# Performance work log

Hardware: AMD Instinct MI355X
Metric: run time of the kernel (lower is better)

The kernel has to match this reference:

```python
import jax, jax.numpy as jnp
import numpy as np

DN = ('NCDHW', 'OIDHW', 'NCDHW')
HIDDEN = 512
VOCAB = 8192


def conv3d_s122(x, w, b):
    # stride (1,2,2), padding 1 on all three spatial-temporal dims
    y = jax.lax.conv_general_dilated(x, w, window_strides=(1, 2, 2),
                                     padding=[(1, 1), (1, 1), (1, 1)],
                                     dimension_numbers=DN)
    return y + b[None, :, None, None, None]


def setup_inputs() -> dict:
    key = jax.random.key(0)
    ks = jax.random.split(key, 9)
    c1, c2 = HIDDEN // 4, HIDDEN // 2
    inp = {
        'video': jax.random.normal(ks[0], (2, 3, 16, 128, 128), dtype=jnp.float32),
        'w1': jax.random.normal(ks[1], (c1, 3, 3, 3, 3), dtype=jnp.float32) * 0.05,
        'b1': jnp.zeros((c1,), dtype=jnp.float32),
        'w2': jax.random.normal(ks[2], (c2, c1, 3, 3, 3), dtype=jnp.float32) * 0.05,
        'b2': jnp.zeros((c2,), dtype=jnp.float32),
        'w3': jax.random.normal(ks[3], (HIDDEN, c2, 3, 3, 3), dtype=jnp.float32) * 0.05,
        'b3': jnp.zeros((HIDDEN,), dtype=jnp.float32),
        'codebook': jax.random.normal(ks[4], (VOCAB, HIDDEN), dtype=jnp.float32),
        'emb_table': jax.random.normal(ks[5], (VOCAB, HIDDEN), dtype=jnp.float32),
        'resolution_level': 0,
    }
    return inp


def reference(video, w1, b1, w2, b2, w3, b3, codebook, emb_table, resolution_level):
    h = jax.nn.relu(conv3d_s122(video, w1, b1))
    h = jax.nn.relu(conv3d_s122(h, w2, b2))
    f = conv3d_s122(h, w3, b3)                       # [B, C, T, H', W']
    B, C = f.shape[0], f.shape[1]
    feats = f.reshape(B, C, -1).transpose(0, 2, 1)   # [B, N, C]
    # squared L2 distances (argmin identical to cdist's sqrt distances)
    f2 = jnp.sum(feats * feats, axis=-1, keepdims=True)          # [B, N, 1]
    c2 = jnp.sum(codebook * codebook, axis=-1)                   # [V]
    dots = jnp.einsum('bnc,vc->bnv', feats, codebook)            # [B, N, V]
    sqdist = f2 + c2[None, None, :] - 2.0 * dots
    tokens = jnp.argmin(sqdist, axis=-1)                         # [B, N] int
    embeddings = emb_table[tokens]                               # [B, N, C]
    return tokens, embeddings
```

## Files before the change

### kernel.cpp

```cpp
#include <hip/hip_runtime.h>

typedef __bf16 bf16x8 __attribute__((ext_vector_type(8)));
typedef float  f32x4  __attribute__((ext_vector_type(4)));

__device__ __forceinline__ unsigned int splitpack(float x) {
  unsigned int u = __float_as_uint(x);
  unsigned int hi = (u + 0x7fffu + ((u >> 16) & 1u)) >> 16;
  float l = x - __uint_as_float(hi << 16);
  unsigned int ul = __float_as_uint(l);
  unsigned int lo = (ul + 0x7fffu + ((ul >> 16) & 1u)) >> 16;
  return hi | (lo << 16);
}

__device__ __forceinline__ void mfma_bf16(f32x4& d, uint4 a, uint4 b) {
  d = __builtin_amdgcn_mfma_f32_16x16x32_bf16(
        __builtin_bit_cast(bf16x8, a), __builtin_bit_cast(bf16x8, b), d, 0, 0, 0);
}

__device__ __forceinline__ void glds16(const void* g, void* l) {
  __builtin_amdgcn_global_load_lds(
      (const __attribute__((address_space(1))) unsigned int*)g,
      (__attribute__((address_space(3))) unsigned int*)l, 16, 0, 0);
}


__global__ void conv1_k(const float* __restrict__ in, const float* __restrict__ wgt,
                        const float* __restrict__ bias,
                        unsigned short* __restrict__ h1h, unsigned short* __restrict__ h1l) {
  const int tx = threadIdx.x;
  const int w0 = tx * 4;
  const int h  = blockIdx.x * 16 + threadIdx.y;
  const int co0 = blockIdx.y * 8;
  const int bz = blockIdx.z;
  const int b = bz >> 4, t = bz & 15;

  float acc[8][4];
  #pragma unroll
  for (int i = 0; i < 8; ++i) {
    const float bv = bias[co0 + i];
    #pragma unroll
    for (int j = 0; j < 4; ++j) acc[i][j] = bv;
  }
  const int cs = 2 * w0 - 2;

  for (int ci = 0; ci < 3; ++ci) {
    const float* inc = in + (size_t)((b * 3 + ci) * 16) * (128 * 128);
    const float* wc  = wgt + ((size_t)co0 * 3 + ci) * 27;
    #pragma unroll
    for (int kd = 0; kd < 3; ++kd) {
      const int t2 = t - 1 + kd;
      if (t2 < 0 || t2 >= 16) continue;
      const float* ip = inc + t2 * (128 * 128);
      #pragma unroll
      for (int kh = 0; kh < 3; ++kh) {
        const int hh = 2 * h - 1 + kh;
        float v[10];
        if (hh >= 0) {
          const float* r = ip + hh * 128 + cs;
          if (cs >= 0) { float2 u = *(const float2*)r; v[0] = u.x; v[1] = u.y; }
          else         { v[0] = 0.f; v[1] = 0.f; }
          float2 u1 = *(const float2*)(r + 2); v[2] = u1.x; v[3] = u1.y;
          float2 u2 = *(const float2*)(r + 4); v[4] = u2.x; v[5] = u2.y;
          float2 u3 = *(const float2*)(r + 6); v[6] = u3.x; v[7] = u3.y;
          float2 u4 = *(const float2*)(r + 8); v[8] = u4.x; v[9] = u4.y;
        } else {
          #pragma unroll
          for (int z = 0; z < 10; ++z) v[z] = 0.f;
        }
        #pragma unroll
        for (int i = 0; i < 8; ++i) {
          const float* wp = wc + (size_t)i * (3 * 27) + kd * 9 + kh * 3;
          const float wa = wp[0], wb = wp[1], wcc = wp[2];
          #pragma unroll
          for (int wi = 0; wi < 4; ++wi) {
            acc[i][wi] = fmaf(v[1 + 2*wi], wa,  acc[i][wi]);
            acc[i][wi] = fmaf(v[2 + 2*wi], wb,  acc[i][wi]);
            acc[i][wi] = fmaf(v[3 + 2*wi], wcc, acc[i][wi]);
          }
        }
      }
    }
  }
  const int ph = h & 1, rr = h >> 1, cc0 = tx * 2;
  const size_t base0 = (size_t)b * 8388608 + (size_t)blockIdx.y * 524288
                     + (size_t)t * 32768 + (size_t)(ph * 2) * 8192 + (size_t)rr * 256;
  #pragma unroll
  for (int pos = 0; pos < 4; ++pos) {
    const size_t idx = base0 + ((pos & 1) ? 8192 : 0) + (size_t)(cc0 + (pos >> 1)) * 8;
    unsigned int hw[4], lw[4];
    #pragma unroll
    for (int ii = 0; ii < 4; ++ii) {
      unsigned int pa = splitpack(fmaxf(acc[2*ii][pos], 0.f));
      unsigned int pb = splitpack(fmaxf(acc[2*ii+1][pos], 0.f));
      hw[ii] = (pa & 0xffffu) | ((pb & 0xffffu) << 16);
      lw[ii] = (pa >> 16) | (pb & 0xffff0000u);
    }
    *(uint4*)(h1h + idx) = make_uint4(hw[0], hw[1], hw[2], hw[3]);
    *(uint4*)(h1l + idx) = make_uint4(lw[0], lw[1], lw[2], lw[3]);
  }
}

__global__ void split_w2_k(const float* __restrict__ w2, unsigned short* __restrict__ whi,
                           unsigned short* __restrict__ wlo) {
  unsigned int o = blockIdx.x * 256u + threadIdx.x;
  unsigned int j   = o & 7u;
  unsigned int col = (o >> 3) & 127u;
  unsigned int kg  = (o >> 10) & 3u;
  unsigned int cbk = (o >> 12) & 1u;
  unsigned int cic = (o >> 13) & 3u;
  unsigned int tap = o >> 15;
  unsigned int co = cbk * 128u + col, ci = cic * 32u + kg * 8u + j;
  float x = w2[((size_t)co * 128u + ci) * 27u + tap];
  unsigned int p = splitpack(x);
  whi[o] = (unsigned short)(p & 0xffffu);
  wlo[o] = (unsigned short)(p >> 16);
}

__global__ void split_w3_k(const float* __restrict__ w3, unsigned short* __restrict__ whi,
                           unsigned short* __restrict__ wlo) {
  unsigned int o = blockIdx.x * 256u + threadIdx.x;
  unsigned int j   = o & 7u;
  unsigned int col = (o >> 3) & 127u;
  unsigned int kg  = (o >> 10) & 3u;
  unsigned int cb  = (o >> 12) & 3u;
  unsigned int cic = (o >> 14) & 7u;
  unsigned int tap = o >> 17;
  unsigned int co = cb * 128u + col, ci = cic * 32u + kg * 8u + j;
  float x = w3[((size_t)co * 256u + ci) * 27u + tap];
  unsigned int p = splitpack(x);
  whi[o] = (unsigned short)(p & 0xffffu);
  wlo[o] = (unsigned short)(p >> 16);
}

__global__ void split_cb_k(const float* __restrict__ cb, unsigned short* __restrict__ cbhi,
                           unsigned short* __restrict__ cblo) {
  unsigned int o = blockIdx.x * 256u + threadIdx.x;
  unsigned int j   = o & 7u;
  unsigned int row = (o >> 3) & 127u;
  unsigned int kq  = (o >> 10) & 3u;
  unsigned int kc  = (o >> 12) & 15u;
  unsigned int vb  = o >> 16;
  unsigned int v = vb * 128u + row, k = kc * 32u + kq * 8u + j;
  float x = cb[(size_t)v * 512u + k];
  unsigned int p = splitpack(x);
  cbhi[o] = (unsigned short)(p & 0xffffu);
  cblo[o] = (unsigned short)(p >> 16);
}

__global__ void c2_k(const float* __restrict__ cb, float* __restrict__ c2) {
  const int wid = threadIdx.x >> 6, lane = threadIdx.x & 63;
  const int v = blockIdx.x * 4 + wid;
  const float* row = cb + (size_t)v * 512 + lane * 8;
  float4 a = *(const float4*)row, b = *(const float4*)(row + 4);
  float s = a.x*a.x + a.y*a.y + a.z*a.z + a.w*a.w
          + b.x*b.x + b.y*b.y + b.z*b.z + b.w*b.w;
  #pragma unroll
  for (int off = 32; off; off >>= 1) s += __shfl_down(s, off);
  if (lane == 0) c2[v] = s;
}

__global__ void zero16_k(unsigned int* __restrict__ p) { p[threadIdx.x] = 0u; }

#define NCH2 108
#define BUFO 16384
__global__ __launch_bounds__(512) void conv2_mfma_k(
    const unsigned short* __restrict__ xh, const unsigned short* __restrict__ xl,
    const unsigned short* __restrict__ whi, const unsigned short* __restrict__ wlo,
    const unsigned short* __restrict__ zp,
    const float* __restrict__ bias,
    unsigned short* __restrict__ h2h, unsigned short* __restrict__ h2l) {
  __shared__ __align__(16) unsigned short lds[32768];

  const int tid  = threadIdx.x;
  const int lane = tid & 63;
  const int wid  = tid >> 6;
  const int wm   = wid >> 2, wn = wid & 3;
  const int bid = blockIdx.x;
  const int xcd = bid & 7;
  const int q   = bid >> 3;
  const int cbk = q & 1;
  const int nb  = (q >> 1) & 7;
  const int bt  = xcd + 8 * (q >> 4);
  const int b = bt >> 4, t = bt & 15;

  const int skg = tid >> 7;
  const int sn  = tid & 127;
  const int s_hout = nb * 4 + (sn >> 5);
  const int s_wout = sn & 31;

  const int lc = lane & 15, kgl = lane >> 4;

  f32x4 acc[4][2];
  #pragma unroll
  for (int mf = 0; mf < 4; ++mf)
    #pragma unroll
    for (int nf = 0; nf < 2; ++nf) acc[mf][nf] = (f32x4)(0.f);

  auto issue = [&](int ic, int bo) {
    const int tap = ic >> 2, cic = ic & 3;
    const int kd = tap / 9, r9 = tap % 9;
    const int kh = r9 / 3, kw = r9 % 3;
    const int tt = t + kd - 1;
    const int pl = ((kh != 1) ? 2 : 0) + ((kw != 1) ? 1 : 0);
    const int r  = s_hout + (kh != 0) - 1;
    const int c  = s_wout + (kw != 0) - 1;
    const bool oob = (tt < 0) || (tt > 15) || (r < 0) || (c < 0);
    const int o = b * 8388608 + (cic * 4 + skg) * 524288 + tt * 32768 + pl * 8192 + (r * 32 + c) * 8;
    const size_t slab = ((size_t)((tap * 4 + cic) * 2 + cbk)) << 12;
    glds16(whi + slab + tid * 8, &lds[bo + tid * 8]);
    glds16(wlo + slab + tid * 8, &lds[bo + 4096 + tid * 8]);
    const unsigned short* sh = oob ? zp : (xh + o);
    const unsigned short* sl = oob ? zp : (xl + o);
    glds16(sh, &lds[bo + 8192 + tid * 8]);
    glds16(sl, &lds[bo + 12288 + tid * 8]);
  };

  auto mma = [&](int bo) {
    uint4 ah[4], al[4], bh[2], bl[2];
    #pragma unroll
    for (int mf = 0; mf < 4; ++mf) {
      const int o = bo + kgl * 1024 + (wm * 64 + mf * 16 + lc) * 8;
      ah[mf] = *(const uint4*)&lds[o];
      al[mf] = *(const uint4*)&lds[o + 4096];
    }
    #pragma unroll
    for (int nf = 0; nf < 2; ++nf) {
      const int o = bo + 8192 + kgl * 1024 + (wn * 32 + nf * 16 + lc) * 8;
      bh[nf] = *(const uint4*)&lds[o];
      bl[nf] = *(const uint4*)&lds[o + 4096];
    }
    #pragma unroll
    for (int mf = 0; mf < 4; ++mf)
      #pragma unroll
      for (int nf = 0; nf < 2; ++nf) mfma_bf16(acc[mf][nf], ah[mf], bh[nf]);
    #pragma unroll
    for (int mf = 0; mf < 4; ++mf)
      #pragma unroll
      for (int nf = 0; nf < 2; ++nf) mfma_bf16(acc[mf][nf], ah[mf], bl[nf]);
    #pragma unroll
    for (int mf = 0; mf < 4; ++mf)
      #pragma unroll
      for (int nf = 0; nf < 2; ++nf) mfma_bf16(acc[mf][nf], al[mf], bh[nf]);
  };

  issue(0, 0);
  #pragma unroll 1
  for (int ic = 0; ic < NCH2; ic += 2) {
    __syncthreads();
    if (ic + 1 < NCH2) issue(ic + 1, BUFO);
    mma(0);
    __syncthreads();
    if (ic + 2 < NCH2) issue(ic + 2, 0);
    mma(BUFO);
  }

  const int lr4 = (lane >> 4) * 4;
  #pragma unroll
  for (int mf = 0; mf < 4; ++mf) {
    const int co0g = cbk * 128 + wm * 64 + mf * 16 + lr4;
    const float4 bv = *(const float4*)(bias + co0g);
    const float* bp = (const float*)&bv;
    const size_t gbase = (size_t)(b * 32 + (co0g >> 3)) * 131072 + (size_t)t * 8192 + (co0g & 7);
    #pragma unroll
    for (int nf = 0; nf < 2; ++nf) {
      const int n_l = wn * 32 + nf * 16 + lc;
      const int h_out = nb * 4 + (n_l >> 5);
      const int w_out = n_l & 31;
      const int pl_o = ((h_out & 1) << 1) | (w_out & 1);
      const size_t sp = gbase + (size_t)pl_o * 2048 + (size_t)((h_out >> 1) * 16 + (w_out >> 1)) * 8;
      unsigned int qv[4];
      #pragma unroll
      for (int r = 0; r < 4; ++r) qv[r] = splitpack(fmaxf(acc[mf][nf][r] + bp[r], 0.f));
      ushort4 h4 = make_ushort4((unsigned short)(qv[0] & 0xffffu), (unsigned short)(qv[1] & 0xffffu),
                                (unsigned short)(qv[2] & 0xffffu), (unsigned short)(qv[3] & 0xffffu));
      ushort4 l4 = make_ushort4((unsigned short)(qv[0] >> 16), (unsigned short)(qv[1] >> 16),
                                (unsigned short)(qv[2] >> 16), (unsigned short)(qv[3] >> 16));
      *(ushort4*)(h2h + sp) = h4;
      *(ushort4*)(h2l + sp) = l4;
    }
  }
}

#define NCH 216
__global__ __launch_bounds__(512) void conv3_mfma_k(
    const unsigned short* __restrict__ xh, const unsigned short* __restrict__ xl,
    const unsigned short* __restrict__ whi, const unsigned short* __restrict__ wlo,
    const unsigned short* __restrict__ zp,
    const float* __restrict__ bias,
    unsigned short* __restrict__ fhi, unsigned short* __restrict__ flo) {
  __shared__ __align__(16) unsigned short lds[32768];

  const int tid  = threadIdx.x;
  const int lane = tid & 63;
  const int wid  = tid >> 6;
  const int wm   = wid >> 2, wn = wid & 3;
  const int bid = blockIdx.x;
  const int xcd = bid & 7;
  const int q   = bid >> 3;
  const int cb  = q & 3;
  const int hb  = (q >> 2) & 1;
  const int bt  = xcd + 8 * (q >> 3);
  const int b = bt >> 4, t = bt & 15;

  const int skg = tid >> 7;
  const int sn  = tid & 127;
  const int shn = hb * 8 + (sn >> 4);
  const int swn = sn & 15;

  const int lc = lane & 15, kgl = lane >> 4;

  f32x4 acc[4][2];
  #pragma unroll
  for (int mf = 0; mf < 4; ++mf)
    #pragma unroll
    for (int nf = 0; nf < 2; ++nf) acc[mf][nf] = (f32x4)(0.f);

  auto issue = [&](int ic, int bo) {
    const int tap = ic >> 3, cic = ic & 7;
    const int kd = tap / 9, r9 = tap % 9;
    const int kh = r9 / 3, kw = r9 % 3;
    const int tt = t + kd - 1;
    const int pl = ((kh != 1) ? 2 : 0) + ((kw != 1) ? 1 : 0);
    const int r  = shn + (kh != 0) - 1;
    const int c  = swn + (kw != 0) - 1;
    const bool oob = (tt < 0) || (tt > 15) || (r < 0) || (c < 0);
    const int o = b * 4194304 + (cic * 4 + skg) * 131072 + tt * 8192 + pl * 2048 + (r * 16 + c) * 8;
    const size_t slab = ((size_t)((tap * 8 + cic) * 4 + cb)) << 12;
    glds16(whi + slab + tid * 8, &lds[bo + tid * 8]);
    glds16(wlo + slab + tid * 8, &lds[bo + 4096 + tid * 8]);
    const unsigned short* sh = oob ? zp : (xh + o);
    const unsigned short* sl = oob ? zp : (xl + o);
    glds16(sh, &lds[bo + 8192 + tid * 8]);
    glds16(sl, &lds[bo + 12288 + tid * 8]);
  };

  auto mma = [&](int bo) {
    uint4 ah[4], al[4], bh[2], bl[2];
    #pragma unroll
    for (int mf = 0; mf < 4; ++mf) {
      const int o = bo + kgl * 1024 + (wm * 64 + mf * 16 + lc) * 8;
      ah[mf] = *(const uint4*)&lds[o];
      al[mf] = *(const uint4*)&lds[o + 4096];
    }
    #pragma unroll
    for (int nf = 0; nf < 2; ++nf) {
      const int o = bo + 8192 + kgl * 1024 + (wn * 32 + nf * 16 + lc) * 8;
      bh[nf] = *(const uint4*)&lds[o];
      bl[nf] = *(const uint4*)&lds[o + 4096];
    }
    #pragma unroll
    for (int mf = 0; mf < 4; ++mf)
      #pragma unroll
      for (int nf = 0; nf < 2; ++nf) mfma_bf16(acc[mf][nf], ah[mf], bh[nf]);
    #pragma unroll
    for (int mf = 0; mf < 4; ++mf)
      #pragma unroll
      for (int nf = 0; nf < 2; ++nf) mfma_bf16(acc[mf][nf], ah[mf], bl[nf]);
    #pragma unroll
    for (int mf = 0; mf < 4; ++mf)
      #pragma unroll
      for (int nf = 0; nf < 2; ++nf) mfma_bf16(acc[mf][nf], al[mf], bh[nf]);
  };

  issue(0, 0);
  #pragma unroll 1
  for (int ic = 0; ic < NCH; ic += 2) {
    __syncthreads();
    if (ic + 1 < NCH) issue(ic + 1, BUFO);
    mma(0);
    __syncthreads();
    if (ic + 2 < NCH) issue(ic + 2, 0);
    mma(BUFO);
  }

  const int lr4 = (lane >> 4) * 4;
  const int tokb = b * 32 + t * 2 + hb;
  #pragma unroll
  for (int mf = 0; mf < 4; ++mf) {
    const int co0g = cb * 128 + wm * 64 + mf * 16 + lr4;
    const float4 bv = *(const float4*)(bias + co0g);
    const int kc = co0g >> 5, kq = (co0g >> 3) & 3, j0 = co0g & 7;
    #pragma unroll
    for (int nf = 0; nf < 2; ++nf) {
      const int n_l = wn * 32 + nf * 16 + lc;
      const size_t off = (size_t)(tokb * 16 + kc) * 4096 + kq * 1024 + n_l * 8 + j0;
      unsigned int p0 = splitpack(acc[mf][nf][0] + bv.x);
      unsigned int p1 = splitpack(acc[mf][nf][1] + bv.y);
      unsigned int p2 = splitpack(acc[mf][nf][2] + bv.z);
      unsigned int p3 = splitpack(acc[mf][nf][3] + bv.w);
      ushort4 h4, l4;
      h4.x = (unsigned short)(p0 & 0xffffu); l4.x = (unsigned short)(p0 >> 16);
      h4.y = (unsigned short)(p1 & 0xffffu); l4.y = (unsigned short)(p1 >> 16);
      h4.z = (unsigned short)(p2 & 0xffffu); l4.z = (unsigned short)(p2 >> 16);
      h4.w = (unsigned short)(p3 & 0xffffu); l4.w = (unsigned short)(p3 >> 16);
      *(ushort4*)(fhi + off) = h4;
      *(ushort4*)(flo + off) = l4;
    }
  }
}

__global__ __launch_bounds__(512) void vq_mfma_k(
    const unsigned short* __restrict__ fhi, const unsigned short* __restrict__ flo,
    const unsigned short* __restrict__ cbhi, const unsigned short* __restrict__ cblo,
    const float* __restrict__ c2,
    float* __restrict__ pval, int* __restrict__ pidx) {
  __shared__ __align__(16) unsigned short lds[32768];

  const int tid  = threadIdx.x;
  const int lane = tid & 63;
  const int wid  = tid >> 6;
  const int wm   = wid >> 2, wn = wid & 3;
  const int vb = blockIdx.x;
  const int tb = blockIdx.y;
  const int v0 = vb * 128, tok0 = tb * 128;

  const int lc = lane & 15, kgl = lane >> 4;

  f32x4 acc[4][2];
  #pragma unroll
  for (int mf = 0; mf < 4; ++mf)
    #pragma unroll
    for (int nf = 0; nf < 2; ++nf) acc[mf][nf] = (f32x4)(0.f);

  auto issue = [&](int kc, int bo) {
    const size_t cboff = (size_t)(vb * 16 + kc) * 4096 + tid * 8;
    const size_t foff  = (size_t)(tb * 16 + kc) * 4096 + tid * 8;
    glds16(cbhi + cboff, &lds[bo + tid * 8]);
    glds16(cblo + cboff, &lds[bo + 4096 + tid * 8]);
    glds16(fhi + foff,  &lds[bo + 8192 + tid * 8]);
    glds16(flo + foff,  &lds[bo + 12288 + tid * 8]);
  };

  auto mma = [&](int bo) {
    uint4 ah[4], al[4], bh[2], bl[2];
    #pragma unroll
    for (int mf = 0; mf < 4; ++mf) {
      const int o = bo + kgl * 1024 + (wm * 64 + mf * 16 + lc) * 8;
      ah[mf] = *(const uint4*)&lds[o];
      al[mf] = *(const uint4*)&lds[o + 4096];
    }
    #pragma unroll
    for (int nf = 0; nf < 2; ++nf) {
      const int o = bo + 8192 + kgl * 1024 + (wn * 32 + nf * 16 + lc) * 8;
      bh[nf] = *(const uint4*)&lds[o];
      bl[nf] = *(const uint4*)&lds[o + 4096];
    }
    #pragma unroll
    for (int mf = 0; mf < 4; ++mf)
      #pragma unroll
      for (int nf = 0; nf < 2; ++nf) mfma_bf16(acc[mf][nf], ah[mf], bh[nf]);
    #pragma unroll
    for (int mf = 0; mf < 4; ++mf)
      #pragma unroll
      for (int nf = 0; nf < 2; ++nf) mfma_bf16(acc[mf][nf], ah[mf], bl[nf]);
    #pragma unroll
    for (int mf = 0; mf < 4; ++mf)
      #pragma unroll
      for (int nf = 0; nf < 2; ++nf) mfma_bf16(acc[mf][nf], al[mf], bh[nf]);
  };

  issue(0, 0);
  #pragma unroll 1
  for (int kc = 0; kc < 16; kc += 2) {
    __syncthreads();
    if (kc + 1 < 16) issue(kc + 1, BUFO);
    mma(0);
    __syncthreads();
    if (kc + 2 < 16) issue(kc + 2, 0);
    mma(BUFO);
  }

  float best[2]; int bidx[2];
  best[0] = best[1] = 3.4e38f; bidx[0] = bidx[1] = 0;
  #pragma unroll
  for (int mf = 0; mf < 4; ++mf) {
    float cc[4];
    *(float4*)cc = *(const float4*)(c2 + v0 + wm * 64 + mf * 16 + kgl * 4);
    #pragma unroll
    for (int nf = 0; nf < 2; ++nf) {
      #pragma unroll
      for (int r = 0; r < 4; ++r) {
        const float d = cc[r] - 2.f * acc[mf][nf][r];
        const int vg = v0 + wm * 64 + mf * 16 + kgl * 4 + r;
        if (d < best[nf] || (d == best[nf] && vg < bidx[nf])) { best[nf] = d; bidx[nf] = vg; }
      }
    }
  }
  #pragma unroll
  for (int off = 16; off <= 32; off <<= 1) {
    #pragma unroll
    for (int nf = 0; nf < 2; ++nf) {
      const float ov = __shfl_xor(best[nf], off);
      const int   oi = __shfl_xor(bidx[nf], off);
      if (ov < best[nf] || (ov == best[nf] && oi < bidx[nf])) { best[nf] = ov; bidx[nf] = oi; }
    }
  }
  if (lane < 16) {
    #pragma unroll
    for (int nf = 0; nf < 2; ++nf) {
      const int tok = tok0 + wn * 32 + nf * 16 + lane;
      const int slot = vb * 2 + wm;
      pval[(size_t)tok * 128 + slot] = best[nf];
      pidx[(size_t)tok * 128 + slot] = bidx[nf];
    }
  }
}

__global__ void vq_reduce_k(const float* __restrict__ pval, const int* __restrict__ pidx,
                            int* __restrict__ tokens, float* __restrict__ out_tok) {
  const int tok = blockIdx.x * blockDim.x + threadIdx.x;
  float best = 3.4e38f; int bi = 0;
  for (int s = 0; s < 128; ++s) {
    const float v = pval[(size_t)tok * 128 + s];
    const int idx = pidx[(size_t)tok * 128 + s];
    if (v < best || (v == best && idx < bi)) { best = v; bi = idx; }
  }
  tokens[tok] = bi;
  out_tok[tok] = (float)bi;
}

__global__ void gather_k(const int* __restrict__ tokens, const float* __restrict__ emb,
                         float* __restrict__ out) {
  const int i = blockIdx.x * blockDim.x + threadIdx.x;
  const int n = i >> 7;
  const int c4 = (i & 127) * 4;
  const int tk = tokens[n];
  float4 v = *(const float4*)(emb + (size_t)tk * 512 + c4);
  *(float4*)(out + (size_t)n * 512 + c4) = v;
}

extern "C" void kernel_launch(void* const* d_in, const int* in_sizes, int n_in,
                              void* d_out, int out_size, void* d_ws, size_t ws_size,
                              hipStream_t stream) {
  const float* video = (const float*)d_in[0];
  const float* w1 = (const float*)d_in[1];
  const float* b1 = (const float*)d_in[2];
  const float* w2 = (const float*)d_in[3];
  const float* b2 = (const float*)d_in[4];
  const float* w3 = (const float*)d_in[5];
  const float* b3 = (const float*)d_in[6];
  const float* cb  = (const float*)d_in[7];
  const float* emb = (const float*)d_in[8];

  float* ws = (float*)d_ws;
  unsigned short* h1h = (unsigned short*)ws;
  unsigned short* h1l = (unsigned short*)(ws + 8388608);
  unsigned short* fhi = (unsigned short*)(ws);
  unsigned short* flo = (unsigned short*)(ws + 2097152);
  unsigned short* cbhi = (unsigned short*)(ws + 4194304);
  unsigned short* cblo = (unsigned short*)(ws + 6291456);
  float* c2v  = ws + 8388608;
  float* pval = ws + 8396800;
  int*   pidx = (int*)(ws + 9445376);
  int*   tokens = (int*)(ws + 10493952);
  unsigned short* h2h = (unsigned short*)(ws + 16777216);
  unsigned short* h2l = (unsigned short*)(ws + 20971520);
  unsigned short* zp  = (unsigned short*)(ws + 25165824);
  unsigned short* w2hi = (unsigned short*)d_out;
  unsigned short* w2lo = w2hi + 884736;
  unsigned short* w3hi = (unsigned short*)d_out;
  unsigned short* w3lo = w3hi + 3538944;
  float* out_tok = (float*)d_out;
  float* out_emb = (float*)d_out + 8192;

  hipLaunchKernelGGL(conv1_k, dim3(4, 16, 32), dim3(16, 16), 0, stream, video, w1, b1, h1h, h1l);
  hipLaunchKernelGGL(split_w2_k, dim3(3456), dim3(256), 0, stream, w2, w2hi, w2lo);
  hipLaunchKernelGGL(zero16_k, dim3(1), dim3(16), 0, stream, (unsigned int*)zp);
  hipLaunchKernelGGL(conv2_mfma_k, dim3(512), dim3(512), 0, stream,
                     h1h, h1l, w2hi, w2lo, zp, b2, h2h, h2l);
  hipLaunchKernelGGL(split_w3_k, dim3(13824), dim3(256), 0, stream, w3, w3hi, w3lo);
  hipLaunchKernelGGL(split_cb_k, dim3(16384), dim3(256), 0, stream, cb, cbhi, cblo);
  hipLaunchKernelGGL(c2_k, dim3(2048), dim3(256), 0, stream, cb, c2v);
  hipLaunchKernelGGL(conv3_mfma_k, dim3(256), dim3(512), 0, stream,
                     h2h, h2l, w3hi, w3lo, zp, b3, fhi, flo);
  hipLaunchKernelGGL(vq_mfma_k, dim3(64, 64), dim3(512), 0, stream,
                     fhi, flo, cbhi, cblo, c2v, pval, pidx);
  hipLaunchKernelGGL(vq_reduce_k, dim3(32), dim3(256), 0, stream, pval, pidx, tokens, out_tok);
  hipLaunchKernelGGL(gather_k, dim3(4096), dim3(256), 0, stream, tokens, emb, out_emb);
}
```

Baseline: 760.7 us.

## Deepen LDS prefetch pipeline with partial vmcnt waits in three GEMM kernels

Measured after the change: 696.8 us. 1.09x faster.

```diff
diff --git a/kernel.cpp b/kernel.cpp
--- a/kernel.cpp
+++ b/kernel.cpp
@@ -21,6 +21,22 @@
   __builtin_amdgcn_global_load_lds(
       (const __attribute__((address_space(1))) unsigned int*)g,
       (__attribute__((address_space(3))) unsigned int*)l, 16, 0, 0);
+}
+
+__device__ __forceinline__ void wait4_bar() {
+  asm volatile("s_waitcnt vmcnt(4)" ::: "memory");
+  __builtin_amdgcn_sched_barrier(0);
+  __builtin_amdgcn_s_barrier();
+}
+__device__ __forceinline__ void wait0_bar() {
+  asm volatile("s_waitcnt vmcnt(0)" ::: "memory");
+  __builtin_amdgcn_sched_barrier(0);
+  __builtin_amdgcn_s_barrier();
+}
+__device__ __forceinline__ void plain_bar() {
+  __builtin_amdgcn_sched_barrier(0);
+  __builtin_amdgcn_s_barrier();
+  __builtin_amdgcn_sched_barrier(0);
 }
 
 
@@ -244,15 +260,22 @@
   };
 
   issue(0, 0);
+  issue(1, BUFO);
   #pragma unroll 1
-  for (int ic = 0; ic < NCH2; ic += 2) {
-    __syncthreads();
-    if (ic + 1 < NCH2) issue(ic + 1, BUFO);
+  for (int ic = 0; ic < NCH2 - 2; ic += 2) {
+    wait4_bar();
     mma(0);
-    __syncthreads();
-    if (ic + 2 < NCH2) issue(ic + 2, 0);
+    plain_bar();
+    issue(ic + 2, 0);
+    wait4_bar();
     mma(BUFO);
-  }
+    plain_bar();
+    issue(ic + 3, BUFO);
+  }
+  wait4_bar();
+  mma(0);
+  wait0_bar();
+  mma(BUFO);
 
   const int lr4 = (lane >> 4) * 4;
   #pragma unroll
@@ -363,15 +386,22 @@
   };
 
   issue(0, 0);
+  issue(1, BUFO);
   #pragma unroll 1
-  for (int ic = 0; ic < NCH; ic += 2) {
-    __syncthreads();
-    if (ic + 1 < NCH) issue(ic + 1, BUFO);
+  for (int ic = 0; ic < NCH - 2; ic += 2) {
+    wait4_bar();
     mma(0);
-    __syncthreads();
-    if (ic + 2 < NCH) issue(ic + 2, 0);
+    plain_bar();
+    issue(ic + 2, 0);
+    wait4_bar();
     mma(BUFO);
-  }
+    plain_bar();
+    issue(ic + 3, BUFO);
+  }
+  wait4_bar();
+  mma(0);
+  wait0_bar();
+  mma(BUFO);
 
   const int lr4 = (lane >> 4) * 4;
   const int tokb = b * 32 + t * 2 + hb;
@@ -460,15 +490,22 @@
   };
 
   issue(0, 0);
+  issue(1, BUFO);
   #pragma unroll 1
-  for (int kc = 0; kc < 16; kc += 2) {
-    __syncthreads();
-    if (kc + 1 < 16) issue(kc + 1, BUFO);
+  for (int kc = 0; kc < 14; kc += 2) {
+    wait4_bar();
     mma(0);
-    __syncthreads();
-    if (kc + 2 < 16) issue(kc + 2, 0);
+    plain_bar();
+    issue(kc + 2, 0);
+    wait4_bar();
     mma(BUFO);
-  }
+    plain_bar();
+    issue(kc + 3, BUFO);
+  }
+  wait4_bar();
+  mma(0);
+  wait0_bar();
+  mma(BUFO);
 
   float best[2]; int bidx[2];
   best[0] = best[1] = 3.4e38f; bidx[0] = bidx[1] = 0;
```
